# Kernel tuning notes

Measured on AMD Instinct MI355X. Metric: run time of the kernel, lower is better.

## Reference

```python
import jax, jax.numpy as jnp
import numpy as np

S, D, H, F = 4096, 2048, 16, 8192
HD = D // H
EPS = 1e-5


def setup_inputs() -> dict:
    key = jax.random.key(0)
    ks = jax.random.split(key, 16)
    sc_d = 1.0 / np.sqrt(D)
    sc_f = 1.0 / np.sqrt(F)
    return {
        "x": jax.random.normal(ks[0], (S, D), dtype=jnp.float32),
        # stacked per-head projections: [H, D, HD]
        "Wq": jax.random.normal(ks[1], (H, D, HD), dtype=jnp.float32) * sc_d,
        "bq": jax.random.normal(ks[2], (H, HD), dtype=jnp.float32) * 0.01,
        "Wk": jax.random.normal(ks[3], (H, D, HD), dtype=jnp.float32) * sc_d,
        "bk": jax.random.normal(ks[4], (H, HD), dtype=jnp.float32) * 0.01,
        "Wv": jax.random.normal(ks[5], (H, D, HD), dtype=jnp.float32) * sc_d,
        "bv": jax.random.normal(ks[6], (H, HD), dtype=jnp.float32) * 0.01,
        "Wp": jax.random.normal(ks[7], (D, D), dtype=jnp.float32) * sc_d,
        "bp": jax.random.normal(ks[8], (D,), dtype=jnp.float32) * 0.01,
        "W1": jax.random.normal(ks[9], (D, F), dtype=jnp.float32) * sc_d,
        "b1": jax.random.normal(ks[10], (F,), dtype=jnp.float32) * 0.01,
        "W2": jax.random.normal(ks[11], (F, D), dtype=jnp.float32) * sc_f,
        "b2": jax.random.normal(ks[12], (D,), dtype=jnp.float32) * 0.01,
        "gamma": jnp.ones((D,), dtype=jnp.float32),
        "beta": jnp.zeros((D,), dtype=jnp.float32),
    }


def _layernorm(x, gamma, beta):
    mu = jnp.mean(x, axis=-1, keepdims=True)
    var = jnp.var(x, axis=-1, keepdims=True)
    return (x - mu) * jax.lax.rsqrt(var + EPS) * gamma + beta


def reference(x, Wq, bq, Wk, bk, Wv, bv, Wp, bp, W1, b1, W2, b2, gamma, beta):
    residual = x
    # batched per-head projections: [H, S, HD]
    q = jnp.einsum('sd,hde->hse', x, Wq) + bq[:, None, :]
    k = jnp.einsum('sd,hde->hse', x, Wk) + bk[:, None, :]
    v = jnp.einsum('sd,hde->hse', x, Wv) + bv[:, None, :]
    scores = jnp.einsum('hse,hte->hst', q, k) / np.sqrt(HD).astype(np.float32)
    attn = jax.nn.softmax(scores, axis=-1)
    heads = jnp.einsum('hst,hte->hse', attn, v)  # [H, S, HD]
    # concat heads along feature dim (head 0 first): [S, H*HD]
    heads = jnp.transpose(heads, (1, 0, 2)).reshape(S, H * HD)
    out = heads @ Wp + bp
    # residual_attn=True, norm_attn=True
    out = out + residual
    out = _layernorm(out, gamma, beta)
    # feedforward (original forward ends here)
    out = jax.nn.relu(out @ W1 + b1) @ W2 + b2
    return out
```

## Files before the change

### kernel.cpp

```cpp
#include <hip/hip_runtime.h>
#include <hip/hip_bf16.h>
#include <cstdint>
#include <cstddef>

#define S 4096
#define D 2048
#define H 16
#define HD 128
#define F 8192

typedef unsigned short ushort_t;
typedef __attribute__((ext_vector_type(8))) short short8;
typedef __attribute__((ext_vector_type(4))) float floatx4;

__device__ __forceinline__ ushort_t f2bf(float f) {
  union { float f; unsigned u; } v; v.f = f;
  unsigned u = v.u;
  return (ushort_t)((u + 0x7fffu + ((u >> 16) & 1u)) >> 16);
}

__device__ __forceinline__ void async16(void* lds, const void* g) {
  __builtin_amdgcn_global_load_lds(
      (const __attribute__((address_space(1))) unsigned int*)g,
      (__attribute__((address_space(3))) unsigned int*)lds, 16, 0, 0);
}


__global__ void cast_bf16(const float* __restrict__ src, ushort_t* __restrict__ dst, int n4) {
  int i = blockIdx.x * blockDim.x + threadIdx.x;
  if (i < n4) {
    float4 v = ((const float4*)src)[i];
    ushort4 o;
    o.x = f2bf(v.x); o.y = f2bf(v.y); o.z = f2bf(v.z); o.w = f2bf(v.w);
    ((ushort4*)dst)[i] = o;
  }
}

__global__ void build_bqkv(const float* __restrict__ bq, const float* __restrict__ bk,
                           const float* __restrict__ bv, float* __restrict__ bqkv) {
  int n = blockIdx.x * blockDim.x + threadIdx.x;
  if (n < 3 * D) {
    float v;
    if (n < D) v = bq[n];
    else if (n < 2 * D) v = bk[n - D];
    else v = bv[n - 2 * D];
    bqkv[n] = v;
  }
}

__global__ void transpose_f32_bf16(const float* __restrict__ src, ushort_t* __restrict__ dst,
                                   int ldS, int ldD, long srcBatchStride, long dstBatchRows) {
  __shared__ float t[32][33];
  int b = blockIdx.z;
  src += (size_t)b * srcBatchStride;
  dst += (size_t)b * dstBatchRows * ldD;
  int r0 = blockIdx.x * 32, c0 = blockIdx.y * 32;
  int tx = threadIdx.x, ty = threadIdx.y;
#pragma unroll
  for (int i = 0; i < 4; ++i)
    t[ty + i * 8][tx] = src[(size_t)(r0 + ty + i * 8) * ldS + c0 + tx];
  __syncthreads();
#pragma unroll
  for (int i = 0; i < 4; ++i)
    dst[(size_t)(c0 + ty + i * 8) * ldD + r0 + tx] = f2bf(t[tx][ty + i * 8]);
}

__global__ void transpose_bf16(const ushort_t* __restrict__ src, ushort_t* __restrict__ dst,
                               int ldS, int ldD, int colOff) {
  __shared__ ushort_t t[32][33];
  int r0 = blockIdx.x * 32, c0 = blockIdx.y * 32;
  int tx = threadIdx.x, ty = threadIdx.y;
#pragma unroll
  for (int i = 0; i < 4; ++i)
    t[ty + i * 8][tx] = src[(size_t)(r0 + ty + i * 8) * ldS + colOff + c0 + tx];
  __syncthreads();
#pragma unroll
  for (int i = 0; i < 4; ++i)
    dst[(size_t)(c0 + ty + i * 8) * ldD + r0 + tx] = t[tx][ty + i * 8];
}

template <int MODE>
__global__ __launch_bounds__(256, 2)
void gemm_bt(const ushort_t* __restrict__ A, const ushort_t* __restrict__ Bt,
             const float* __restrict__ bias, const float* __restrict__ resid,
             ushort_t* __restrict__ outb, float* __restrict__ outf,
             int M, int N, int K) {
  __shared__ __align__(16) ushort_t As[128 * 32];
  __shared__ __align__(16) ushort_t Bs[128 * 32];
  const int tid = threadIdx.x;
  const int w = tid >> 6, l = tid & 63;
  const int wr = w >> 1, wc = w & 1;
  const int g = l >> 4, c16 = l & 15;
  const int m0 = blockIdx.y * 128, n0 = blockIdx.x * 128;

  floatx4 acc[4][4];
#pragma unroll
  for (int i = 0; i < 4; ++i)
#pragma unroll
    for (int j = 0; j < 4; ++j) acc[i][j] = (floatx4){0.f, 0.f, 0.f, 0.f};

  for (int k0 = 0; k0 < K; k0 += 32) {
#pragma unroll
    for (int c = 0; c < 2; ++c) {
      int flat = (c * 256 + tid) * 16;
      int row = flat >> 6, colb = flat & 63;
      const char* ga = (const char*)A + ((size_t)(m0 + row) * K + k0) * 2 + colb;
      async16((char*)As + (size_t)(c * 256 + w * 64) * 16, ga);
      const char* gb = (const char*)Bt + ((size_t)(n0 + row) * K + k0) * 2 + colb;
      async16((char*)Bs + (size_t)(c * 256 + w * 64) * 16, gb);
    }
    __syncthreads();
    short8 af[4], bf[4];
#pragma unroll
    for (int i = 0; i < 4; ++i)
      af[i] = *(const short8*)(As + (wr * 64 + i * 16 + c16) * 32 + g * 8);
#pragma unroll
    for (int j = 0; j < 4; ++j)
      bf[j] = *(const short8*)(Bs + (wc * 64 + j * 16 + c16) * 32 + g * 8);
#pragma unroll
    for (int i = 0; i < 4; ++i)
#pragma unroll
      for (int j = 0; j < 4; ++j)
        acc[i][j] = __builtin_amdgcn_mfma_f32_16x16x32_bf16(af[i], bf[j], acc[i][j], 0, 0, 0);
    __syncthreads();
  }

#pragma unroll
  for (int j = 0; j < 4; ++j) {
    int gcol = n0 + wc * 64 + j * 16 + c16;
    float bj = bias[gcol];
#pragma unroll
    for (int i = 0; i < 4; ++i) {
      int rbase = m0 + wr * 64 + i * 16 + g * 4;
#pragma unroll
      for (int r = 0; r < 4; ++r) {
        int grow = rbase + r;
        float v = acc[i][j][r] + bj;
        if (MODE == 0) {
          outb[(size_t)grow * N + gcol] = f2bf(v);
        } else if (MODE == 1) {
          outf[(size_t)grow * N + gcol] = v + resid[(size_t)grow * N + gcol];
        } else if (MODE == 2) {
          outb[(size_t)grow * N + gcol] = f2bf(v > 0.f ? v : 0.f);
        } else {
          outf[(size_t)grow * N + gcol] = v;
        }
      }
    }
  }
}

__global__ __launch_bounds__(256, 2)
void attn_kernel(const ushort_t* __restrict__ QKV, const ushort_t* __restrict__ Vt,
                 ushort_t* __restrict__ heads) {
  const int h = blockIdx.y;
  const int tid = threadIdx.x, w = tid >> 6, l = tid & 63;
  const int g = l >> 4, c = l & 15;
  const int q0 = blockIdx.x * 128 + w * 32;
  const float scale = 0.08838834764831845f;

  __shared__ __align__(16) ushort_t Ks[64 * 128];
  __shared__ __align__(16) ushort_t Vs[128 * 64];
  __shared__ __align__(16) ushort_t Ps[4][2][16][72];

  short8 qf[2][4];
#pragma unroll
  for (int u = 0; u < 2; ++u)
#pragma unroll
    for (int k0 = 0; k0 < 4; ++k0)
      qf[u][k0] = *(const short8*)(QKV + (size_t)(q0 + u * 16 + c) * (3 * D) + h * HD + k0 * 32 + g * 8);

  floatx4 o[2][8];
#pragma unroll
  for (int u = 0; u < 2; ++u)
#pragma unroll
    for (int j = 0; j < 8; ++j) o[u][j] = (floatx4){0.f, 0.f, 0.f, 0.f};
  float l_run[2] = {0.f, 0.f};

  for (int t0 = 0; t0 < S; t0 += 64) {
#pragma unroll
    for (int cc = 0; cc < 4; ++cc) {
      int slot = cc * 256 + tid;
      int krow = slot >> 4, kch = slot & 15;
      const char* gk = (const char*)QKV +
          ((size_t)(t0 + krow) * (3 * D) + D + h * HD) * 2 + ((kch ^ (krow & 15)) << 4);
      async16((char*)Ks + (size_t)(cc * 256 + w * 64) * 16, gk);
      int vrow = slot >> 3, vch = slot & 7;
      const char* gv = (const char*)Vt +
          ((size_t)(h * HD + vrow) * S + t0) * 2 + ((vch ^ (vrow & 7)) << 4);
      async16((char*)Vs + (size_t)(cc * 256 + w * 64) * 16, gv);
    }
    __syncthreads();

    floatx4 sc[2][4];
#pragma unroll
    for (int u = 0; u < 2; ++u)
#pragma unroll
      for (int tt = 0; tt < 4; ++tt) sc[u][tt] = (floatx4){0.f, 0.f, 0.f, 0.f};
#pragma unroll
    for (int tt = 0; tt < 4; ++tt) {
      short8 kf[4];
#pragma unroll
      for (int k0 = 0; k0 < 4; ++k0)
        kf[k0] = *(const short8*)(Ks + (tt * 16 + c) * 128 + (((k0 * 4 + g) ^ c) << 3));
#pragma unroll
      for (int u = 0; u < 2; ++u)
#pragma unroll
        for (int k0 = 0; k0 < 4; ++k0)
          sc[u][tt] = __builtin_amdgcn_mfma_f32_16x16x32_bf16(kf[k0], qf[u][k0], sc[u][tt], 0, 0, 0);
    }

#pragma unroll
    for (int u = 0; u < 2; ++u) {
#pragma unroll
      for (int tt = 0; tt < 4; ++tt) {
        float p0 = __expf(sc[u][tt][0] * scale);
        float p1 = __expf(sc[u][tt][1] * scale);
        float p2 = __expf(sc[u][tt][2] * scale);
        float p3 = __expf(sc[u][tt][3] * scale);
        l_run[u] += p0 + p1 + p2 + p3;
        ushort4 pk;
        pk.x = f2bf(p0); pk.y = f2bf(p1); pk.z = f2bf(p2); pk.w = f2bf(p3);
        *reinterpret_cast<ushort4*>(&Ps[w][u][c][tt * 16 + g * 4]) = pk;
      }
    }
    __asm__ volatile("s_waitcnt lgkmcnt(0)" ::: "memory");

    short8 pf[2][2];
#pragma unroll
    for (int u = 0; u < 2; ++u)
#pragma unroll
      for (int tk = 0; tk < 2; ++tk)
        pf[u][tk] = *reinterpret_cast<const short8*>(&Ps[w][u][c][tk * 32 + g * 8]);
#pragma unroll
    for (int j = 0; j < 8; ++j) {
#pragma unroll
      for (int tk = 0; tk < 2; ++tk) {
        short8 vf = *(const short8*)(Vs + (j * 16 + c) * 64 + (((tk * 4 + g) ^ (c & 7)) << 3));
#pragma unroll
        for (int u = 0; u < 2; ++u)
          o[u][j] = __builtin_amdgcn_mfma_f32_16x16x32_bf16(pf[u][tk], vf, o[u][j], 0, 0, 0);
      }
    }
    __syncthreads();
  }

#pragma unroll
  for (int u = 0; u < 2; ++u) {
    float lt = l_run[u];
    lt += __shfl_xor(lt, 16);
    lt += __shfl_xor(lt, 32);
    float linv[4];
#pragma unroll
    for (int r = 0; r < 4; ++r) linv[r] = 1.f / __shfl(lt, g * 4 + r);
    ushort_t* hp = heads + (size_t)(q0 + u * 16 + g * 4) * D + h * HD + c;
#pragma unroll
    for (int j = 0; j < 8; ++j)
#pragma unroll
      for (int r = 0; r < 4; ++r)
        hp[(size_t)r * D + j * 16] = f2bf(o[u][j][r] * linv[r]);
  }
}

__global__ __launch_bounds__(256)
void ln_kernel(const float* __restrict__ preln, const float* __restrict__ gamma,
               const float* __restrict__ beta, ushort_t* __restrict__ y) {
  int row = blockIdx.x, tid = threadIdx.x;
  const float* p = preln + (size_t)row * D;
  float vals[8];
  float sum = 0.f, ss = 0.f;
#pragma unroll
  for (int k = 0; k < 8; ++k) {
    float v = p[tid + k * 256];
    vals[k] = v; sum += v; ss += v * v;
  }
#pragma unroll
  for (int off = 32; off >= 1; off >>= 1) {
    sum += __shfl_xor(sum, off);
    ss += __shfl_xor(ss, off);
  }
  __shared__ float s1[4], s2[4];
  int w = tid >> 6, l = tid & 63;
  if (l == 0) { s1[w] = sum; s2[w] = ss; }
  __syncthreads();
  sum = s1[0] + s1[1] + s1[2] + s1[3];
  ss = s2[0] + s2[1] + s2[2] + s2[3];
  float mu = sum / (float)D;
  float var = ss / (float)D - mu * mu;
  float rs = rsqrtf(var + 1e-5f);
  ushort_t* yr = y + (size_t)row * D;
#pragma unroll
  for (int k = 0; k < 8; ++k) {
    int d = tid + k * 256;
    yr[d] = f2bf((vals[k] - mu) * rs * gamma[d] + beta[d]);
  }
}


extern "C" void kernel_launch(void* const* d_in, const int* in_sizes, int n_in,
                              void* d_out, int out_size, void* d_ws, size_t ws_size,
                              hipStream_t stream) {
  const float* x = (const float*)d_in[0];
  const float* Wq = (const float*)d_in[1];
  const float* bq = (const float*)d_in[2];
  const float* Wk = (const float*)d_in[3];
  const float* bk = (const float*)d_in[4];
  const float* Wv = (const float*)d_in[5];
  const float* bv = (const float*)d_in[6];
  const float* Wp = (const float*)d_in[7];
  const float* bp = (const float*)d_in[8];
  const float* W1 = (const float*)d_in[9];
  const float* b1 = (const float*)d_in[10];
  const float* W2 = (const float*)d_in[11];
  const float* b2 = (const float*)d_in[12];
  const float* gamma = (const float*)d_in[13];
  const float* beta = (const float*)d_in[14];

  char* ws = (char*)d_ws;
  ushort_t* WQKVT = (ushort_t*)(ws + 0);
  ushort_t* XB    = (ushort_t*)(ws + 25165824);
  float*    BQKV  = (float*)(ws + 41943040);
  ushort_t* WPT   = (ushort_t*)(ws + 41975808);
  ushort_t* W1T   = (ushort_t*)(ws + 50364416);
  ushort_t* W2T   = (ushort_t*)(ws + 83918848);
  ushort_t* QKV   = (ushort_t*)(ws + 117473280);
  ushort_t* HEADS = (ushort_t*)(ws + 167804928);
  ushort_t* VT    = (ushort_t*)(ws + 184582144);
  float*    PRELN = (float*)(ws + 0);
  ushort_t* AB    = (ushort_t*)(ws + 117473280);
  ushort_t* Y     = (ushort_t*)(ws + 184582144);
  float* OUT = (float*)d_out;

  dim3 tb(32, 8);
  cast_bf16<<<(S * D / 4 + 255) / 256, 256, 0, stream>>>(x, XB, S * D / 4);
  build_bqkv<<<(3 * D + 255) / 256, 256, 0, stream>>>(bq, bk, bv, BQKV);
  transpose_f32_bf16<<<dim3(D / 32, HD / 32, H), tb, 0, stream>>>(Wq, WQKVT, HD, D, (long)D * HD, HD);
  transpose_f32_bf16<<<dim3(D / 32, HD / 32, H), tb, 0, stream>>>(Wk, WQKVT + (size_t)D * D, HD, D, (long)D * HD, HD);
  transpose_f32_bf16<<<dim3(D / 32, HD / 32, H), tb, 0, stream>>>(Wv, WQKVT + (size_t)2 * D * D, HD, D, (long)D * HD, HD);
  transpose_f32_bf16<<<dim3(D / 32, D / 32, 1), tb, 0, stream>>>(Wp, WPT, D, D, 0, 0);
  transpose_f32_bf16<<<dim3(D / 32, F / 32, 1), tb, 0, stream>>>(W1, W1T, F, D, 0, 0);
  transpose_f32_bf16<<<dim3(F / 32, D / 32, 1), tb, 0, stream>>>(W2, W2T, D, F, 0, 0);
  gemm_bt<0><<<dim3(3 * D / 128, S / 128), 256, 0, stream>>>(XB, WQKVT, BQKV, nullptr, QKV, nullptr, S, 3 * D, D);
  transpose_bf16<<<dim3(S / 32, D / 32), tb, 0, stream>>>(QKV, VT, 3 * D, S, 2 * D);
  attn_kernel<<<dim3(S / 128, H), 256, 0, stream>>>(QKV, VT, HEADS);
  gemm_bt<1><<<dim3(D / 128, S / 128), 256, 0, stream>>>(HEADS, WPT, bp, x, nullptr, PRELN, S, D, D);
  ln_kernel<<<S, 256, 0, stream>>>(PRELN, gamma, beta, Y);
  gemm_bt<2><<<dim3(F / 128, S / 128), 256, 0, stream>>>(Y, W1T, b1, nullptr, AB, nullptr, S, F, D);
  gemm_bt<3><<<dim3(D / 128, S / 128), 256, 0, stream>>>(AB, W2T, b2, nullptr, nullptr, OUT, S, D, F);
}
```

Before: 1.041 ms.

## Replace GEMM with 8-wave double-buffered pipelined kernel with swizzled LDS

Replaces the simple 128x128, K=32 tiled GEMM with a 512-thread kernel using 256-wide N tiles (BM of 128 or 256), K=64 steps, double-buffered LDS with XOR-swizzled layout, and interleaved async loads with MFMA phases controlled by explicit vmcnt waits and barriers. It also remaps workgroup IDs across the 8 XCDs for cache locality and raises MFMA priority. The aim is to hide global load latency, cut LDS bank conflicts, and raise arithmetic intensity per tile. In exchange it uses much more LDS and registers and depends on hand-tuned wait counts being correct.

```diff
diff --git a/kernel.cpp b/kernel.cpp
--- a/kernel.cpp
+++ b/kernel.cpp
@@ -24,6 +24,17 @@
       (const __attribute__((address_space(1))) unsigned int*)g,
       (__attribute__((address_space(3))) unsigned int*)lds, 16, 0, 0);
 }
+
+template <int N>
+__device__ __forceinline__ void vmcnt_() {
+  static_assert(N >= 0 && N <= 4, "vmcnt range");
+  if constexpr (N == 0) asm volatile("s_waitcnt vmcnt(0)" ::: "memory");
+  else if constexpr (N == 1) asm volatile("s_waitcnt vmcnt(1)" ::: "memory");
+  else if constexpr (N == 2) asm volatile("s_waitcnt vmcnt(2)" ::: "memory");
+  else if constexpr (N == 3) asm volatile("s_waitcnt vmcnt(3)" ::: "memory");
+  else asm volatile("s_waitcnt vmcnt(4)" ::: "memory");
+}
+__device__ __forceinline__ void bar_() { asm volatile("s_barrier" ::: "memory"); }
 
 
 __global__ void cast_bf16(const float* __restrict__ src, ushort_t* __restrict__ dst, int n4) {
@@ -79,75 +90,217 @@
     dst[(size_t)(c0 + ty + i * 8) * ldD + r0 + tx] = t[tx][ty + i * 8];
 }
 
-template <int MODE>
-__global__ __launch_bounds__(256, 2)
-void gemm_bt(const ushort_t* __restrict__ A, const ushort_t* __restrict__ Bt,
-             const float* __restrict__ bias, const float* __restrict__ resid,
-             ushort_t* __restrict__ outb, float* __restrict__ outf,
-             int M, int N, int K) {
-  __shared__ __align__(16) ushort_t As[128 * 32];
-  __shared__ __align__(16) ushort_t Bs[128 * 32];
+template <int MODE, int BM>
+__global__ __launch_bounds__(512, 2)
+void gemm8p(const ushort_t* __restrict__ A, const ushort_t* __restrict__ Bt,
+            const float* __restrict__ bias, const float* __restrict__ resid,
+            ushort_t* __restrict__ outb, float* __restrict__ outf,
+            int M, int N, int K, int gridN) {
+  constexpr int MF = BM / 64;
+  constexpr int LA = BM / 128;
+  constexpr int AT = BM * 64;
+  constexpr int BT = 256 * 64;
+  __shared__ __align__(16) ushort_t Abuf[2][AT];
+  __shared__ __align__(16) ushort_t Bbuf[2][BT];
+
   const int tid = threadIdx.x;
-  const int w = tid >> 6, l = tid & 63;
-  const int wr = w >> 1, wc = w & 1;
-  const int g = l >> 4, c16 = l & 15;
-  const int m0 = blockIdx.y * 128, n0 = blockIdx.x * 128;
-
-  floatx4 acc[4][4];
-#pragma unroll
-  for (int i = 0; i < 4; ++i)
-#pragma unroll
-    for (int j = 0; j < 4; ++j) acc[i][j] = (floatx4){0.f, 0.f, 0.f, 0.f};
-
-  for (int k0 = 0; k0 < K; k0 += 32) {
-#pragma unroll
-    for (int c = 0; c < 2; ++c) {
-      int flat = (c * 256 + tid) * 16;
-      int row = flat >> 6, colb = flat & 63;
-      const char* ga = (const char*)A + ((size_t)(m0 + row) * K + k0) * 2 + colb;
-      async16((char*)As + (size_t)(c * 256 + w * 64) * 16, ga);
-      const char* gb = (const char*)Bt + ((size_t)(n0 + row) * K + k0) * 2 + colb;
-      async16((char*)Bs + (size_t)(c * 256 + w * 64) * 16, gb);
-    }
-    __syncthreads();
-    short8 af[4], bf[4];
-#pragma unroll
-    for (int i = 0; i < 4; ++i)
-      af[i] = *(const short8*)(As + (wr * 64 + i * 16 + c16) * 32 + g * 8);
-#pragma unroll
-    for (int j = 0; j < 4; ++j)
-      bf[j] = *(const short8*)(Bs + (wc * 64 + j * 16 + c16) * 32 + g * 8);
-#pragma unroll
-    for (int i = 0; i < 4; ++i)
-#pragma unroll
-      for (int j = 0; j < 4; ++j)
-        acc[i][j] = __builtin_amdgcn_mfma_f32_16x16x32_bf16(af[i], bf[j], acc[i][j], 0, 0, 0);
-    __syncthreads();
-  }
-
-#pragma unroll
-  for (int j = 0; j < 4; ++j) {
-    int gcol = n0 + wc * 64 + j * 16 + c16;
-    float bj = bias[gcol];
-#pragma unroll
-    for (int i = 0; i < 4; ++i) {
-      int rbase = m0 + wr * 64 + i * 16 + g * 4;
-#pragma unroll
-      for (int r = 0; r < 4; ++r) {
-        int grow = rbase + r;
-        float v = acc[i][j][r] + bj;
-        if (MODE == 0) {
-          outb[(size_t)grow * N + gcol] = f2bf(v);
-        } else if (MODE == 1) {
-          outf[(size_t)grow * N + gcol] = v + resid[(size_t)grow * N + gcol];
-        } else if (MODE == 2) {
-          outb[(size_t)grow * N + gcol] = f2bf(v > 0.f ? v : 0.f);
-        } else {
-          outf[(size_t)grow * N + gcol] = v;
+  const int l = tid & 63, w = tid >> 6;
+  const int c16 = l & 15, g = l >> 4;
+  const int wr2 = w >> 2, wc4 = w & 3;
+
+  const int nwg = gridDim.x;
+  const int q8 = nwg >> 3, r8 = nwg & 7;
+  const int xcd = blockIdx.x & 7, bix = blockIdx.x >> 3;
+  const int wgid = (xcd < r8 ? xcd * (q8 + 1) : r8 * (q8 + 1) + (xcd - r8) * q8) + bix;
+  const int m0 = (wgid / gridN) * BM;
+  const int n0 = (wgid % gridN) * 256;
+
+  const size_t Kb = (size_t)K * 2;
+
+  const char* aSrc[LA]; char* aLds[LA];
+#pragma unroll
+  for (int i = 0; i < LA; ++i) {
+    int ch = i * 512 + tid;
+    int row = ch >> 3;
+    int slot = ((ch ^ row) & 7) << 4;
+    aSrc[i] = (const char*)A + (size_t)(m0 + row) * Kb + slot;
+    aLds[i] = (char*)(&Abuf[0][0]) + ch * 16;
+  }
+  const char* bSrc[2]; char* bLds[2];
+#pragma unroll
+  for (int i = 0; i < 2; ++i) {
+    int ch = i * 512 + tid;
+    int row = ch >> 3;
+    int slot = ((ch ^ row) & 7) << 4;
+    bSrc[i] = (const char*)Bt + (size_t)(n0 + row) * Kb + slot;
+    bLds[i] = (char*)(&Bbuf[0][0]) + ch * 16;
+  }
+  const size_t aHalf = (size_t)(BM / 2) * Kb;
+  const size_t bHalf = (size_t)128 * Kb;
+
+  int rdK[2];
+  rdK[0] = ((g ^ (c16 & 7)) << 4);
+  rdK[1] = (((4 + g) ^ (c16 & 7)) << 4);
+  const int aRd = wr2 * (BM / 4) * 128 + c16 * 128;
+  const int bRd = wc4 * 32 * 128 + c16 * 128;
+
+  floatx4 acc[2][2][MF][2];
+#pragma unroll
+  for (int mh = 0; mh < 2; ++mh)
+#pragma unroll
+    for (int nh = 0; nh < 2; ++nh)
+#pragma unroll
+      for (int mf = 0; mf < MF; ++mf)
+#pragma unroll
+        for (int nf = 0; nf < 2; ++nf) acc[mh][nh][mf][nf] = (floatx4){0.f, 0.f, 0.f, 0.f};
+
+  const int NT = K >> 6;
+
+#pragma unroll
+  for (int i = 0; i < LA; ++i) async16(aLds[i], aSrc[i]);
+#pragma unroll
+  for (int i = 0; i < 2; ++i) async16(bLds[i], bSrc[i]);
+#pragma unroll
+  for (int i = 0; i < 2; ++i) async16(bLds[i] + 128 * 128, bSrc[i] + bHalf);
+#pragma unroll
+  for (int i = 0; i < LA; ++i) async16(aLds[i] + (BM / 2) * 128, aSrc[i] + aHalf);
+  vmcnt_<2 + LA>();
+  bar_();
+
+  for (int T = 0; T < NT; ++T) {
+    const int kb = T & 1, kn = kb ^ 1;
+    const bool last = (T == NT - 1);
+    const size_t kOff = (size_t)(T + 1) << 7;
+    const char* ab = (const char*)(&Abuf[0][0]) + kb * (AT * 2);
+    const char* bb = (const char*)(&Bbuf[0][0]) + kb * (BT * 2);
+    const int aOf = kn * (AT * 2), bOf = kn * (BT * 2);
+    short8 af[MF][2], bf0[2][2], bf1[2][2];
+
+#pragma unroll
+    for (int mf = 0; mf < MF; ++mf)
+#pragma unroll
+      for (int kk = 0; kk < 2; ++kk)
+        af[mf][kk] = *(const short8*)(ab + aRd + mf * 2048 + rdK[kk]);
+#pragma unroll
+    for (int nf = 0; nf < 2; ++nf)
+#pragma unroll
+      for (int kk = 0; kk < 2; ++kk)
+        bf0[nf][kk] = *(const short8*)(bb + bRd + nf * 2048 + rdK[kk]);
+    if (!last) {
+#pragma unroll
+      for (int i = 0; i < LA; ++i) async16(aLds[i] + aOf, aSrc[i] + kOff);
+    }
+    bar_();
+    __builtin_amdgcn_s_setprio(1);
+#pragma unroll
+    for (int mf = 0; mf < MF; ++mf)
+#pragma unroll
+      for (int nf = 0; nf < 2; ++nf)
+#pragma unroll
+        for (int kk = 0; kk < 2; ++kk)
+          acc[0][0][mf][nf] = __builtin_amdgcn_mfma_f32_16x16x32_bf16(
+              af[mf][kk], bf0[nf][kk], acc[0][0][mf][nf], 0, 0, 0);
+    __builtin_amdgcn_s_setprio(0);
+    __builtin_amdgcn_sched_barrier(0);
+    if (!last) vmcnt_<2 * LA>(); else vmcnt_<LA>();
+    bar_();
+
+#pragma unroll
+    for (int nf = 0; nf < 2; ++nf)
+#pragma unroll
+      for (int kk = 0; kk < 2; ++kk)
+        bf1[nf][kk] = *(const short8*)(bb + bRd + 16384 + nf * 2048 + rdK[kk]);
+    if (!last) {
+#pragma unroll
+      for (int i = 0; i < 2; ++i) async16(bLds[i] + bOf, bSrc[i] + kOff);
+    }
+    bar_();
+    __builtin_amdgcn_s_setprio(1);
+#pragma unroll
+    for (int mf = 0; mf < MF; ++mf)
+#pragma unroll
+      for (int nf = 0; nf < 2; ++nf)
+#pragma unroll
+        for (int kk = 0; kk < 2; ++kk)
+          acc[0][1][mf][nf] = __builtin_amdgcn_mfma_f32_16x16x32_bf16(
+              af[mf][kk], bf1[nf][kk], acc[0][1][mf][nf], 0, 0, 0);
+    __builtin_amdgcn_s_setprio(0);
+    __builtin_amdgcn_sched_barrier(0);
+    if (!last) vmcnt_<LA + 2>(); else vmcnt_<0>();
+    bar_();
+
+#pragma unroll
+    for (int mf = 0; mf < MF; ++mf)
+#pragma unroll
+      for (int kk = 0; kk < 2; ++kk)
+        af[mf][kk] = *(const short8*)(ab + aRd + (BM / 2) * 128 + mf * 2048 + rdK[kk]);
+    if (!last) {
+#pragma unroll
+      for (int i = 0; i < 2; ++i) async16(bLds[i] + bOf + 16384, bSrc[i] + bHalf + kOff);
+    }
+    bar_();
+    __builtin_amdgcn_s_setprio(1);
+#pragma unroll
+    for (int mf = 0; mf < MF; ++mf)
+#pragma unroll
+      for (int nf = 0; nf < 2; ++nf)
+#pragma unroll
+        for (int kk = 0; kk < 2; ++kk)
+          acc[1][1][mf][nf] = __builtin_amdgcn_mfma_f32_16x16x32_bf16(
+              af[mf][kk], bf1[nf][kk], acc[1][1][mf][nf], 0, 0, 0);
+    __builtin_amdgcn_s_setprio(0);
+    __builtin_amdgcn_sched_barrier(0);
+    bar_();
+
+    if (!last) {
+#pragma unroll
+      for (int i = 0; i < LA; ++i) async16(aLds[i] + aOf + (BM / 2) * 128, aSrc[i] + aHalf + kOff);
+    }
+    bar_();
+    __builtin_amdgcn_s_setprio(1);
+#pragma unroll
+    for (int mf = 0; mf < MF; ++mf)
+#pragma unroll
+      for (int nf = 0; nf < 2; ++nf)
+#pragma unroll
+        for (int kk = 0; kk < 2; ++kk)
+          acc[1][0][mf][nf] = __builtin_amdgcn_mfma_f32_16x16x32_bf16(
+              af[mf][kk], bf0[nf][kk], acc[1][0][mf][nf], 0, 0, 0);
+    __builtin_amdgcn_s_setprio(0);
+    __builtin_amdgcn_sched_barrier(0);
+    if (!last) vmcnt_<2 + LA>();
+    bar_();
+  }
+
+  const int mBase = m0 + wr2 * (BM / 4) + g * 4;
+  const int nBase = n0 + wc4 * 32 + c16;
+#pragma unroll
+  for (int mh = 0; mh < 2; ++mh)
+#pragma unroll
+    for (int nh = 0; nh < 2; ++nh)
+#pragma unroll
+      for (int nf = 0; nf < 2; ++nf) {
+        int gcol = nBase + nh * 128 + nf * 16;
+        float bj = bias[gcol];
+#pragma unroll
+        for (int mf = 0; mf < MF; ++mf) {
+          int grow = mBase + mh * (BM / 2) + mf * 16;
+#pragma unroll
+          for (int r = 0; r < 4; ++r) {
+            float v = acc[mh][nh][mf][nf][r] + bj;
+            size_t o = (size_t)(grow + r) * N + gcol;
+            if (MODE == 0) {
+              outb[o] = f2bf(v);
+            } else if (MODE == 1) {
+              outf[o] = v + resid[o];
+            } else if (MODE == 2) {
+              outb[o] = f2bf(v > 0.f ? v : 0.f);
+            } else {
+              outf[o] = v;
+            }
+          }
         }
       }
-    }
-  }
 }
 
 __global__ __launch_bounds__(256, 2)
@@ -340,11 +493,15 @@
   transpose_f32_bf16<<<dim3(D / 32, D / 32, 1), tb, 0, stream>>>(Wp, WPT, D, D, 0, 0);
   transpose_f32_bf16<<<dim3(D / 32, F / 32, 1), tb, 0, stream>>>(W1, W1T, F, D, 0, 0);
   transpose_f32_bf16<<<dim3(F / 32, D / 32, 1), tb, 0, stream>>>(W2, W2T, D, F, 0, 0);
-  gemm_bt<0><<<dim3(3 * D / 128, S / 128), 256, 0, stream>>>(XB, WQKVT, BQKV, nullptr, QKV, nullptr, S, 3 * D, D);
+  gemm8p<0, 256><<<dim3((S / 256) * (3 * D / 256)), 512, 0, stream>>>(
+      XB, WQKVT, BQKV, nullptr, QKV, nullptr, S, 3 * D, D, 3 * D / 256);
   transpose_bf16<<<dim3(S / 32, D / 32), tb, 0, stream>>>(QKV, VT, 3 * D, S, 2 * D);
   attn_kernel<<<dim3(S / 128, H), 256, 0, stream>>>(QKV, VT, HEADS);
-  gemm_bt<1><<<dim3(D / 128, S / 128), 256, 0, stream>>>(HEADS, WPT, bp, x, nullptr, PRELN, S, D, D);
+  gemm8p<1, 128><<<dim3((S / 128) * (D / 256)), 512, 0, stream>>>(
+      HEADS, WPT, bp, x, nullptr, PRELN, S, D, D, D / 256);
   ln_kernel<<<S, 256, 0, stream>>>(PRELN, gamma, beta, Y);
-  gemm_bt<2><<<dim3(F / 128, S / 128), 256, 0, stream>>>(Y, W1T, b1, nullptr, AB, nullptr, S, F, D);
-  gemm_bt<3><<<dim3(D / 128, S / 128), 256, 0, stream>>>(AB, W2T, b2, nullptr, nullptr, OUT, S, D, F);
-}
+  gemm8p<2, 256><<<dim3((S / 256) * (F / 256)), 512, 0, stream>>>(
+      Y, W1T, b1, nullptr, AB, nullptr, S, F, D, F / 256);
+  gemm8p<3, 128><<<dim3((S / 128) * (D / 256)), 512, 0, stream>>>(
+      AB, W2T, b2, nullptr, nullptr, OUT, S, D, F, D / 256);
+}
```

New measurement: 959.0 us. -7.8%, faster.
